# Kernel tuning notes

Hardware: AMD Instinct MI355X
Metric: run time of the kernel (lower is better)

The kernel has to match this reference:

```python
import jax, jax.numpy as jnp
import numpy as np

N_NODES, N_EDGES, N_GRAPHS = 100000, 800000, 64
X_DIM, E_DIM, U_DIM, H = 128, 64, 128, 128
BN_EPS = 1e-5


def _bn(x, gamma, beta):
    # BatchNorm1d, training mode: biased batch stats over dim 0
    m = x.mean(axis=0)
    v = x.var(axis=0)
    return (x - m) * jax.lax.rsqrt(v + BN_EPS) * gamma + beta


def _mlp(x, Wa, ba, g, be, Wb, bb):
    h = jax.nn.selu(_bn(x @ Wa + ba, g, be))
    return h @ Wb + bb


def setup_inputs() -> dict:
    key = jax.random.key(0)
    ks = jax.random.split(key, 10)
    x = jax.random.normal(ks[0], (N_NODES, X_DIM), jnp.float32)
    edge_attr = jax.random.normal(ks[1], (N_EDGES, E_DIM), jnp.float32)
    u = jax.random.normal(ks[2], (N_GRAPHS, U_DIM), jnp.float32)
    edge_index = jax.random.randint(ks[3], (2, N_EDGES), 0, N_NODES, jnp.int32)
    batch = jnp.sort(jax.random.randint(ks[4], (N_NODES,), 0, N_GRAPHS, jnp.int32))

    def lin(k, fan_in, fan_out):
        return jax.random.normal(k, (fan_in, fan_out), jnp.float32) / np.sqrt(fan_in)

    return {
        "x": x, "edge_attr": edge_attr, "u": u,
        "W1a": lin(ks[5], X_DIM + E_DIM, H), "b1a": jnp.zeros(H),
        "g1": jnp.ones(H), "be1": jnp.zeros(H),
        "W1b": lin(ks[6], H, H), "b1b": jnp.zeros(H),
        "W2a": lin(ks[7], X_DIM + H + U_DIM, H), "b2a": jnp.zeros(H),
        "g2": jnp.ones(H), "be2": jnp.zeros(H),
        "W2b": lin(ks[8], H, H), "b2b": jnp.zeros(H),
        "edge_index": edge_index, "batch": batch,
    }


def reference(x, edge_attr, u, W1a, b1a, g1, be1, W1b, b1b,
              W2a, b2a, g2, be2, W2b, b2b, edge_index, batch):
    row, col = edge_index[0], edge_index[1]
    n = x.shape[0]
    # gather source node feats, run edge MLP
    out = jnp.concatenate([x[row], edge_attr], axis=1)        # [E, X+Ed]
    out = _mlp(out, W1a, b1a, g1, be1, W1b, b1b)              # [E, H]
    # scatter-mean over destination nodes
    s = jax.ops.segment_sum(out, col, num_segments=n)         # [N, H]
    cnt = jax.ops.segment_sum(jnp.ones((out.shape[0], 1), out.dtype), col,
                              num_segments=n)
    agg = s / jnp.maximum(cnt, 1.0)
    # node update MLP
    out2 = jnp.concatenate([x, agg, u[batch]], axis=1)        # [N, X+H+U]
    return _mlp(out2, W2a, b2a, g2, be2, W2b, b2b)
```

## Files before the change

### kernel.cpp

```cpp
#include <hip/hip_runtime.h>
#include <hip/hip_bf16.h>
#include <math.h>


typedef __attribute__((ext_vector_type(8))) short bfrag;
typedef __attribute__((ext_vector_type(4))) float f32x4;
typedef __attribute__((ext_vector_type(4))) float f4raw;
typedef __attribute__((ext_vector_type(2))) unsigned u32x2;

#define N_EDGES 800000
#define N_NODES 100000
#define BN_EPS 1e-5f

static __device__ __forceinline__ short f2bf(float f) {
    union { float f; unsigned u; } v; v.f = f;
    unsigned r = (v.u + 0x7FFFu + ((v.u >> 16) & 1u)) >> 16;
    return (short)r;
}
static __device__ __forceinline__ float bf2f(short h) {
    union { unsigned u; float f; } v;
    v.u = ((unsigned)(unsigned short)h) << 16;
    return v.f;
}
static __device__ __forceinline__ unsigned pack2(float lo, float hi) {
    return ((unsigned)(unsigned short)f2bf(lo)) | (((unsigned)(unsigned short)f2bf(hi)) << 16);
}

static __device__ __forceinline__ bfrag load8f_bf(const float* __restrict__ p) {
    float4 a = *(const float4*)p;
    float4 b = *(const float4*)(p + 4);
    bfrag r;
    r[0] = f2bf(a.x); r[1] = f2bf(a.y); r[2] = f2bf(a.z); r[3] = f2bf(a.w);
    r[4] = f2bf(b.x); r[5] = f2bf(b.y); r[6] = f2bf(b.z); r[7] = f2bf(b.w);
    return r;
}
static __device__ __forceinline__ bfrag load8f_bf_nt(const float* __restrict__ p) {
    f4raw a = __builtin_nontemporal_load((const f4raw*)p);
    f4raw b = __builtin_nontemporal_load((const f4raw*)(p + 4));
    bfrag r;
    r[0] = f2bf(a[0]); r[1] = f2bf(a[1]); r[2] = f2bf(a[2]); r[3] = f2bf(a[3]);
    r[4] = f2bf(b[0]); r[5] = f2bf(b[1]); r[6] = f2bf(b[2]); r[7] = f2bf(b[3]);
    return r;
}
static __device__ __forceinline__ u32x2 ldnt_u2(const short* p) {
    return __builtin_nontemporal_load((const u32x2*)p);
}
static __device__ __forceinline__ void stnt_frag(short* p, bfrag v) {
    __builtin_nontemporal_store(v, (bfrag*)p);
}

static __device__ __forceinline__ float selu_f(float v) {
    return v > 0.f ? 1.0507009873554805f * v
                   : 1.7580993408473766f * (__expf(v) - 1.0f);
}

static __device__ __forceinline__ void pack_slot(short* __restrict__ Wp, int k, int n, float val) {
    int kb = k >> 5, g = (k >> 3) & 3, j = k & 7;
    Wp[(((size_t)kb * 128 + n) * 4 + g) * 8 + j] = f2bf(val);
}

__global__ void prep(const float* __restrict__ W1a, const float* __restrict__ W1b,
                     const float* __restrict__ b1b, const float* __restrict__ W2a,
                     const float* __restrict__ W2b,
                     short* __restrict__ Wp1x, short* __restrict__ Wp1e,
                     short* __restrict__ Wp2a, short* __restrict__ Wp2b,
                     float* __restrict__ cb,
                     const int* __restrict__ colI, int* __restrict__ CNTi, int E)
{
    const int b = blockIdx.x, t = threadIdx.x;
    if (b < 64) {
        int idx = b * 256 + t; int k = idx >> 7, n = idx & 127;
        pack_slot(Wp1x, k, n, W1a[idx]);
    } else if (b < 96) {
        int idx = (b - 64) * 256 + t; int k = idx >> 7, n = idx & 127;
        pack_slot(Wp1e, k, n, W1a[128 * 128 + idx]);
    } else if (b < 160) {
        int idx = (b - 96) * 256 + t; int k = idx >> 7, n = idx & 127;
        pack_slot(Wp2a, k, n, W2a[idx]);
    } else if (b < 224) {
        int idx = (b - 160) * 256 + t; int k = idx >> 7, n = idx & 127;
        int kt = ((k & 7) << 4) + (k >> 3);
        float s = 0.f;
        for (int j = 0; j < 128; ++j)
            s += W1b[kt * 128 + j] * W2a[(size_t)(128 + j) * 128 + n];
        pack_slot(Wp2a + 16384, k, n, s);
    } else if (b < 288) {
        int idx = (b - 224) * 256 + t; int k = idx >> 7, n = idx & 127;
        pack_slot(Wp2a + 32768, k, n, W2a[(size_t)256 * 128 + idx]);
    } else if (b < 352) {
        int idx = (b - 288) * 256 + t; int k = idx >> 7, n = idx & 127;
        int kt = ((k & 7) << 4) + (k >> 3);
        pack_slot(Wp2b, k, n, W2b[(size_t)kt * 128 + n]);
    } else if (b == 352) {
        if (t < 128) {
            float s = 0.f;
            for (int j = 0; j < 128; ++j) s += b1b[j] * W2a[(size_t)(128 + j) * 128 + t];
            cb[t] = s;
        }
    } else {
        int e = (b - 353) * 256 + t;
        if (e < E) atomicAdd(&CNTi[colI[e]], 1);
    }
}

__global__ void scan1(const int* __restrict__ cnt, int* __restrict__ off,
                      int* __restrict__ bsum, int N) {
    __shared__ int ls[1024];
    int i = blockIdx.x * 1024 + threadIdx.x;
    int v = (i < N) ? cnt[i] : 0;
    ls[threadIdx.x] = v;
    __syncthreads();
    for (int d = 1; d < 1024; d <<= 1) {
        int t = (threadIdx.x >= d) ? ls[threadIdx.x - d] : 0;
        __syncthreads();
        ls[threadIdx.x] += t;
        __syncthreads();
    }
    if (i < N) off[i] = ls[threadIdx.x] - v;
    if (threadIdx.x == 1023) bsum[blockIdx.x] = ls[1023];
}

__global__ void scan2(const int* __restrict__ bsum, int* __restrict__ boff, int NB) {
    __shared__ int ls[128];
    int v = (threadIdx.x < NB) ? bsum[threadIdx.x] : 0;
    ls[threadIdx.x] = v;
    __syncthreads();
    for (int d = 1; d < 128; d <<= 1) {
        int t = (threadIdx.x >= d) ? ls[threadIdx.x - d] : 0;
        __syncthreads();
        ls[threadIdx.x] += t;
        __syncthreads();
    }
    if (threadIdx.x < NB) boff[threadIdx.x] = ls[threadIdx.x] - v;
}

__global__ void scan3(int* __restrict__ off, const int* __restrict__ boff, int N) {
    int i = blockIdx.x * 1024 + threadIdx.x;
    if (i < N) off[i] += boff[blockIdx.x];
}

__global__ void fill_k(const int* __restrict__ col, int* __restrict__ off,
                       int* __restrict__ spos, int E) {
    int e = blockIdx.x * 256 + threadIdx.x;
    if (e < E) spos[e] = atomicAdd(&off[col[e]], 1);
}

__global__ __launch_bounds__(256) void gemmX(
    const float* __restrict__ x, const short* __restrict__ Wp,
    short* __restrict__ Xap, int N)
{
    const int lane = threadIdx.x & 63, wave = threadIdx.x >> 6;
    const int m0 = blockIdx.x * 128 + wave * 32;
    if (m0 >= N) return;
    const int lr = lane & 15, lg = lane >> 4;
    const int v0 = m0 + lr, v1 = m0 + 16 + lr;

    f32x4 acc[2][8];
#pragma unroll
    for (int t = 0; t < 2; ++t)
#pragma unroll
        for (int n = 0; n < 8; ++n) acc[t][n] = (f32x4){0.f, 0.f, 0.f, 0.f};

#pragma unroll
    for (int kb = 0; kb < 4; ++kb) {
        bfrag a0 = load8f_bf(x + (size_t)v0 * 128 + kb * 32 + lg * 8);
        bfrag a1 = load8f_bf(x + (size_t)v1 * 128 + kb * 32 + lg * 8);
        const short* wb = Wp + (size_t)kb * 4096;
#pragma unroll
        for (int n0 = 0; n0 < 8; ++n0) {
            bfrag b = *(const bfrag*)(wb + ((n0 * 16 + lr) * 4 + lg) * 8);
            acc[0][n0] = __builtin_amdgcn_mfma_f32_16x16x32_bf16(a0, b, acc[0][n0], 0, 0, 0);
            acc[1][n0] = __builtin_amdgcn_mfma_f32_16x16x32_bf16(a1, b, acc[1][n0], 0, 0, 0);
        }
    }
#pragma unroll
    for (int t = 0; t < 2; ++t) {
        const int rbase = m0 + t * 16 + lg * 4;
#pragma unroll
        for (int r = 0; r < 4; ++r) {
            bfrag o;
#pragma unroll
            for (int n0 = 0; n0 < 8; ++n0) o[n0] = f2bf(acc[t][n0][r]);
            *(bfrag*)(Xap + (size_t)(rbase + r) * 128 + lr * 8) = o;
        }
    }
}

__global__ __launch_bounds__(256) void gemm1n(
    const float* __restrict__ ea, const int* __restrict__ rowI,
    const int* __restrict__ SPOS, const short* __restrict__ Wp,
    const short* __restrict__ Xap, short* __restrict__ T1p,
    float* __restrict__ stats, int E)
{
    const int lane = threadIdx.x & 63, wave = threadIdx.x >> 6;
    const int lr = lane & 15, lg = lane >> 4;

    float ps[8], qs[8];
#pragma unroll
    for (int n0 = 0; n0 < 8; ++n0) { ps[n0] = 0.f; qs[n0] = 0.f; }

    const int NT = E >> 7;
    for (int tile = blockIdx.x; tile < NT; tile += gridDim.x) {
        const int m0 = tile * 128 + wave * 32;

        int spos[2][4];
        bfrag xa[2][4];
#pragma unroll
        for (int t = 0; t < 2; ++t) {
            const int rbase = m0 + t * 16 + lg * 4;
#pragma unroll
            for (int r = 0; r < 4; ++r) {
                const int e = rbase + r;
                spos[t][r] = SPOS[e];
                xa[t][r] = *(const bfrag*)(Xap + (size_t)rowI[e] * 128 + lr * 8);
            }
        }

        const float* er0 = ea + (size_t)(m0 + lr) * 64;
        const float* er1 = ea + (size_t)(m0 + 16 + lr) * 64;

        f32x4 acc[2][8];
#pragma unroll
        for (int t = 0; t < 2; ++t)
#pragma unroll
            for (int n = 0; n < 8; ++n) acc[t][n] = (f32x4){0.f, 0.f, 0.f, 0.f};

#pragma unroll
        for (int kb = 0; kb < 2; ++kb) {
            bfrag a0 = load8f_bf_nt(er0 + kb * 32 + lg * 8);
            bfrag a1 = load8f_bf_nt(er1 + kb * 32 + lg * 8);
            const short* wb = Wp + (size_t)kb * 4096;
#pragma unroll
            for (int n0 = 0; n0 < 8; ++n0) {
                bfrag b = *(const bfrag*)(wb + ((n0 * 16 + lr) * 4 + lg) * 8);
                acc[0][n0] = __builtin_amdgcn_mfma_f32_16x16x32_bf16(a0, b, acc[0][n0], 0, 0, 0);
                acc[1][n0] = __builtin_amdgcn_mfma_f32_16x16x32_bf16(a1, b, acc[1][n0], 0, 0, 0);
            }
        }

#pragma unroll
        for (int t = 0; t < 2; ++t) {
#pragma unroll
            for (int r = 0; r < 4; ++r) {
                bfrag o;
#pragma unroll
                for (int n0 = 0; n0 < 8; ++n0) {
                    float v = acc[t][n0][r] + bf2f(xa[t][r][n0]);
                    ps[n0] += v; qs[n0] += v * v;
                    o[n0] = f2bf(v);
                }
                stnt_frag(T1p + (size_t)spos[t][r] * 128 + lr * 8, o);
            }
        }
    }

    __shared__ float ls[256];
    ls[threadIdx.x] = 0.f;
    __syncthreads();
#pragma unroll
    for (int n0 = 0; n0 < 8; ++n0) {
        const int c = n0 * 16 + lr;
        float p = ps[n0], q = qs[n0];
        p += __shfl_xor(p, 16); p += __shfl_xor(p, 32);
        q += __shfl_xor(q, 16); q += __shfl_xor(q, 32);
        if (lg == 0) { atomicAdd(&ls[c], p); atomicAdd(&ls[128 + c], q); }
    }
    __syncthreads();
    atomicAdd(&stats[threadIdx.x], ls[threadIdx.x]);
}

__global__ __launch_bounds__(256) void gemm3f(
    const float* __restrict__ x, const short* __restrict__ T1p,
    const float* __restrict__ stats1, const float* __restrict__ g1,
    const float* __restrict__ be1,
    const int* __restrict__ OFF, const int* __restrict__ CNTi,
    const float* __restrict__ u, const int* __restrict__ batch,
    const float* __restrict__ cb, const short* __restrict__ Wp,
    short* __restrict__ T2p, float* __restrict__ stats2,
    int N, float invE)
{
    __shared__ short aggL[128][136];
    __shared__ float ls[256];
    __shared__ float ls_sc[128], ls_sh[128];
    ls[threadIdx.x] = 0.f;
    if (threadIdx.x < 128) {
        int p = threadIdx.x;
        int c = ((p & 7) << 4) + (p >> 3);
        float mean = stats1[c] * invE;
        float var = stats1[128 + c] * invE - mean * mean;
        float sc = g1[c] * rsqrtf(var + BN_EPS);
        ls_sc[p] = sc;
        ls_sh[p] = be1[c] - mean * sc;
    }
    __syncthreads();

    const int lane = threadIdx.x & 63, wave = threadIdx.x >> 6;
    const int m0b = blockIdx.x * 128;

    {
        const int h = lane >> 5, t = lane & 31;
        const float sc0 = ls_sc[t * 4 + 0], sc1 = ls_sc[t * 4 + 1];
        const float sc2 = ls_sc[t * 4 + 2], sc3 = ls_sc[t * 4 + 3];
        const float sh0 = ls_sh[t * 4 + 0], sh1 = ls_sh[t * 4 + 1];
        const float sh2 = ls_sh[t * 4 + 2], sh3 = ls_sh[t * 4 + 3];
        for (int i = 0; i < 32; ++i) {
            const int v = m0b + wave * 32 + i;
            if (v >= N) break;
            const int cnt = CNTi[v];
            const int beg = OFF[v] - cnt;
            const short* base = T1p + (size_t)beg * 128 + t * 4;
            float a0 = 0.f, a1 = 0.f, a2 = 0.f, a3 = 0.f;
            int j = 0;
            for (; j + 4 <= cnt; j += 4) {
                u32x2 wA = ldnt_u2(base + (size_t)(j + h) * 128);
                u32x2 wB = ldnt_u2(base + (size_t)(j + 2 + h) * 128);
                a0 += selu_f(sc0 * bf2f((short)(wA[0] & 0xffff)) + sh0);
                a1 += selu_f(sc1 * bf2f((short)(wA[0] >> 16)) + sh1);
                a2 += selu_f(sc2 * bf2f((short)(wA[1] & 0xffff)) + sh2);
                a3 += selu_f(sc3 * bf2f((short)(wA[1] >> 16)) + sh3);
                a0 += selu_f(sc0 * bf2f((short)(wB[0] & 0xffff)) + sh0);
                a1 += selu_f(sc1 * bf2f((short)(wB[0] >> 16)) + sh1);
                a2 += selu_f(sc2 * bf2f((short)(wB[1] & 0xffff)) + sh2);
                a3 += selu_f(sc3 * bf2f((short)(wB[1] >> 16)) + sh3);
            }
            for (; j < cnt; j += 2) {
                if (j + h < cnt) {
                    u32x2 w = ldnt_u2(base + (size_t)(j + h) * 128);
                    a0 += selu_f(sc0 * bf2f((short)(w[0] & 0xffff)) + sh0);
                    a1 += selu_f(sc1 * bf2f((short)(w[0] >> 16)) + sh1);
                    a2 += selu_f(sc2 * bf2f((short)(w[1] & 0xffff)) + sh2);
                    a3 += selu_f(sc3 * bf2f((short)(w[1] >> 16)) + sh3);
                }
            }
            a0 += __shfl_xor(a0, 32); a1 += __shfl_xor(a1, 32);
            a2 += __shfl_xor(a2, 32); a3 += __shfl_xor(a3, 32);
            if (h == 0) {
                const float inv = 1.0f / fmaxf((float)cnt, 1.0f);
                u32x2 o;
                o[0] = pack2(a0 * inv, a1 * inv);
                o[1] = pack2(a2 * inv, a3 * inv);
                *(u32x2*)&aggL[wave * 32 + i][t * 4] = o;
            }
        }
    }
    __syncthreads();

    const int m0 = m0b + wave * 32;
    const bool active = (m0 < N);
    const int lr = lane & 15, lg = lane >> 4;

    if (active) {
        const int v0 = m0 + lr, v1 = m0 + 16 + lr;
        const float* u0 = u + (size_t)batch[v0] * 128;
        const float* u1 = u + (size_t)batch[v1] * 128;

        f32x4 acc[2][8];
#pragma unroll
        for (int t = 0; t < 2; ++t)
#pragma unroll
            for (int n = 0; n < 8; ++n) acc[t][n] = (f32x4){0.f, 0.f, 0.f, 0.f};

#pragma unroll
        for (int kb = 0; kb < 12; ++kb) {
            bfrag a0, a1;
            if (kb >= 4 && kb < 8) {
                a0 = *(const bfrag*)&aggL[wave * 32 + lr][(kb - 4) * 32 + lg * 8];
                a1 = *(const bfrag*)&aggL[wave * 32 + 16 + lr][(kb - 4) * 32 + lg * 8];
            } else {
                const float *p0, *p1;
                if (kb < 4) {
                    p0 = x + (size_t)v0 * 128 + kb * 32 + lg * 8;
                    p1 = x + (size_t)v1 * 128 + kb * 32 + lg * 8;
                } else {
                    p0 = u0 + (kb - 8) * 32 + lg * 8;
                    p1 = u1 + (kb - 8) * 32 + lg * 8;
                }
                a0 = load8f_bf(p0);
                a1 = load8f_bf(p1);
            }
            const short* wb = Wp + (size_t)kb * 4096;
#pragma unroll
            for (int n0 = 0; n0 < 8; ++n0) {
                bfrag b = *(const bfrag*)(wb + ((n0 * 16 + lr) * 4 + lg) * 8);
                acc[0][n0] = __builtin_amdgcn_mfma_f32_16x16x32_bf16(a0, b, acc[0][n0], 0, 0, 0);
                acc[1][n0] = __builtin_amdgcn_mfma_f32_16x16x32_bf16(a1, b, acc[1][n0], 0, 0, 0);
            }
        }
        float cbl[8];
#pragma unroll
        for (int n0 = 0; n0 < 8; ++n0) cbl[n0] = cb[n0 * 16 + lr];
        float ps[8], qs[8];
#pragma unroll
        for (int n0 = 0; n0 < 8; ++n0) { ps[n0] = 0.f; qs[n0] = 0.f; }
#pragma unroll
        for (int t = 0; t < 2; ++t) {
            const int rbase = m0 + t * 16 + lg * 4;
            float fl[4];
#pragma unroll
            for (int r = 0; r < 4; ++r) fl[r] = (CNTi[rbase + r] > 0) ? 1.f : 0.f;
#pragma unroll
            for (int r = 0; r < 4; ++r) {
                bfrag o;
#pragma unroll
                for (int n0 = 0; n0 < 8; ++n0) {
                    float v = acc[t][n0][r] + fl[r] * cbl[n0];
                    ps[n0] += v; qs[n0] += v * v;
                    o[n0] = f2bf(v);
                }
                *(bfrag*)(T2p + (size_t)(rbase + r) * 128 + lr * 8) = o;
            }
        }
#pragma unroll
        for (int n0 = 0; n0 < 8; ++n0) {
            const int c = n0 * 16 + lr;
            float p = ps[n0], q = qs[n0];
            p += __shfl_xor(p, 16); p += __shfl_xor(p, 32);
            q += __shfl_xor(q, 16); q += __shfl_xor(q, 32);
            if (lg == 0) { atomicAdd(&ls[c], p); atomicAdd(&ls[128 + c], q); }
        }
    }
    __syncthreads();
    atomicAdd(&stats2[threadIdx.x], ls[threadIdx.x]);
}

__global__ __launch_bounds__(256) void gemm4_node(
    const short* __restrict__ T2p, const float* __restrict__ stats,
    const float* __restrict__ g2, const float* __restrict__ be2,
    const short* __restrict__ Wp, const float* __restrict__ b2b,
    float* __restrict__ out, int N, float invR)
{
    __shared__ float ls_sc[128], ls_sh[128];
    if (threadIdx.x < 128) {
        int c = threadIdx.x;
        float mean = stats[c] * invR;
        float var = stats[128 + c] * invR - mean * mean;
        float sc = g2[c] * rsqrtf(var + BN_EPS);
        ls_sc[c] = sc;
        ls_sh[c] = be2[c] - mean * sc;
    }
    __syncthreads();

    const int lane = threadIdx.x & 63, wave = threadIdx.x >> 6;
    const int m0 = blockIdx.x * 128 + wave * 32;
    if (m0 >= N) return;
    const int lr = lane & 15, lg = lane >> 4;
    const int e0 = m0 + lr, e1 = m0 + 16 + lr;

    f32x4 acc[2][8];
#pragma unroll
    for (int n0 = 0; n0 < 8; ++n0) {
        float bias = b2b[n0 * 16 + lr];
        acc[0][n0] = (f32x4){bias, bias, bias, bias};
        acc[1][n0] = (f32x4){bias, bias, bias, bias};
    }
#pragma unroll
    for (int kb = 0; kb < 4; ++kb) {
        float scl[8], shf[8];
#pragma unroll
        for (int j = 0; j < 8; ++j) {
            int c = j * 16 + kb * 4 + lg;
            scl[j] = ls_sc[c];
            shf[j] = ls_sh[c];
        }
        bfrag r0 = *(const bfrag*)(T2p + (size_t)e0 * 128 + kb * 32 + lg * 8);
        bfrag r1 = *(const bfrag*)(T2p + (size_t)e1 * 128 + kb * 32 + lg * 8);
        bfrag a0, a1;
#pragma unroll
        for (int j = 0; j < 8; ++j) {
            a0[j] = f2bf(selu_f(bf2f(r0[j]) * scl[j] + shf[j]));
            a1[j] = f2bf(selu_f(bf2f(r1[j]) * scl[j] + shf[j]));
        }
        const short* wb = Wp + (size_t)kb * 4096;
#pragma unroll
        for (int n0 = 0; n0 < 8; ++n0) {
            bfrag b = *(const bfrag*)(wb + ((n0 * 16 + lr) * 4 + lg) * 8);
            acc[0][n0] = __builtin_amdgcn_mfma_f32_16x16x32_bf16(a0, b, acc[0][n0], 0, 0, 0);
            acc[1][n0] = __builtin_amdgcn_mfma_f32_16x16x32_bf16(a1, b, acc[1][n0], 0, 0, 0);
        }
    }
#pragma unroll
    for (int t = 0; t < 2; ++t) {
        const int rbase = m0 + t * 16 + lg * 4;
#pragma unroll
        for (int n0 = 0; n0 < 8; ++n0) {
            const int c = n0 * 16 + lr;
#pragma unroll
            for (int r = 0; r < 4; ++r)
                __builtin_nontemporal_store(acc[t][n0][r],
                    out + (size_t)(rbase + r) * 128 + c);
        }
    }
}

extern "C" void kernel_launch(void* const* d_in, const int* in_sizes, int n_in,
                              void* d_out, int out_size, void* d_ws, size_t ws_size,
                              hipStream_t stream)
{
    const float* x   = (const float*)d_in[0];
    const float* ea  = (const float*)d_in[1];
    const float* u   = (const float*)d_in[2];
    const float* W1a = (const float*)d_in[3];
    const float* g1  = (const float*)d_in[5];
    const float* be1 = (const float*)d_in[6];
    const float* W1b = (const float*)d_in[7];
    const float* b1b = (const float*)d_in[8];
    const float* W2a = (const float*)d_in[9];
    const float* g2  = (const float*)d_in[11];
    const float* be2 = (const float*)d_in[12];
    const float* W2b = (const float*)d_in[13];
    const float* b2b = (const float*)d_in[14];
    const int* ei    = (const int*)d_in[15];
    const int* rowI  = ei;
    const int* colI  = ei + N_EDGES;
    const int* batch = (const int*)d_in[16];
    float* out = (float*)d_out;

    if (ws_size < 260252416ull) return;

    char* ws = (char*)d_ws;
    short* Wp1x   = (short*)(ws + 0);
    short* Wp1e   = (short*)(ws + 32768);
    short* Wp2a   = (short*)(ws + 49152);
    short* Wp2b   = (short*)(ws + 147456);
    float* cb     = (float*)(ws + 245760);
    float* stats1 = (float*)(ws + 246272);
    float* stats2 = (float*)(ws + 247296);
    int*   CNTi   = (int*)(ws + 250368);
    int*   OFF    = (int*)(ws + 650368);
    int*   BSUM   = (int*)(ws + 1050368);
    int*   BOFF   = (int*)(ws + 1051392);
    int*   SPOS   = (int*)(ws + 1052416);
    short* Xap    = (short*)(ws + 29852416ull);
    short* T2p    = (short*)(ws + 29852416ull);
    short* T1p    = (short*)(ws + 55452416ull);

    hipMemsetAsync(stats1, 0, 2048, stream);
    hipMemsetAsync(CNTi, 0, 400000, stream);

    prep<<<353 + (N_EDGES + 255) / 256, 256, 0, stream>>>(
        W1a, W1b, b1b, W2a, W2b, Wp1x, Wp1e, Wp2a, Wp2b, cb, colI, CNTi, N_EDGES);

    scan1<<<98, 1024, 0, stream>>>(CNTi, OFF, BSUM, N_NODES);
    scan2<<<1, 128, 0, stream>>>(BSUM, BOFF, 98);
    scan3<<<98, 1024, 0, stream>>>(OFF, BOFF, N_NODES);
    fill_k<<<(N_EDGES + 255) / 256, 256, 0, stream>>>(colI, OFF, SPOS, N_EDGES);

    gemmX<<<(N_NODES + 127) / 128, 256, 0, stream>>>(x, Wp1x, Xap, N_NODES);

    gemm1n<<<2048, 256, 0, stream>>>(ea, rowI, SPOS, Wp1e, Xap, T1p, stats1, N_EDGES);

    gemm3f<<<(N_NODES + 127) / 128, 256, 0, stream>>>(
        x, T1p, stats1, g1, be1, OFF, CNTi, u, batch, cb, Wp2a, T2p, stats2,
        N_NODES, 1.0f / (float)N_EDGES);

    gemm4_node<<<(N_NODES + 127) / 128, 256, 0, stream>>>(T2p, stats2, g2, be2, Wp2b, b2b,
                                                          out, N_NODES, 1.0f / (float)N_NODES);
}
```

Before: 458.3 us.

## Split segment aggregation out of node GEMM into separate wide-grid kernel

The fused gemm3f kernel did the segment-mean aggregation (BN+SELU over T1 rows) in LDS and then ran the node GEMM. This splits it into segsel, a 2048-block kernel that writes per-node means to a global bf16 buffer, and gemm3_node, which reads that buffer as the A operand. The aim is more parallelism for the memory-bound gather phase, since the old launch had only 782 blocks doing 32 serial nodes per wave. The cost is an extra kernel launch and a 25.6MB write plus read-back of the aggregate buffer.

Measured after the change: 370.7 us (median of 2 runs). 19.1% less time.

```diff
diff --git a/kernel.cpp b/kernel.cpp
--- a/kernel.cpp
+++ b/kernel.cpp
@@ -269,85 +269,90 @@
     atomicAdd(&stats[threadIdx.x], ls[threadIdx.x]);
 }
 
-__global__ __launch_bounds__(256) void gemm3f(
-    const float* __restrict__ x, const short* __restrict__ T1p,
-    const float* __restrict__ stats1, const float* __restrict__ g1,
-    const float* __restrict__ be1,
+__global__ __launch_bounds__(256) void segsel(
+    const short* __restrict__ T1p, const float* __restrict__ stats,
+    const float* __restrict__ g1, const float* __restrict__ be1,
     const int* __restrict__ OFF, const int* __restrict__ CNTi,
-    const float* __restrict__ u, const int* __restrict__ batch,
-    const float* __restrict__ cb, const short* __restrict__ Wp,
-    short* __restrict__ T2p, float* __restrict__ stats2,
-    int N, float invE)
-{
-    __shared__ short aggL[128][136];
-    __shared__ float ls[256];
+    short* __restrict__ Aggm, int N, float invR)
+{
     __shared__ float ls_sc[128], ls_sh[128];
-    ls[threadIdx.x] = 0.f;
     if (threadIdx.x < 128) {
         int p = threadIdx.x;
         int c = ((p & 7) << 4) + (p >> 3);
-        float mean = stats1[c] * invE;
-        float var = stats1[128 + c] * invE - mean * mean;
+        float mean = stats[c] * invR;
+        float var = stats[128 + c] * invR - mean * mean;
         float sc = g1[c] * rsqrtf(var + BN_EPS);
         ls_sc[p] = sc;
         ls_sh[p] = be1[c] - mean * sc;
     }
     __syncthreads();
 
+    const int lane = threadIdx.x & 63;
+    const int h = lane >> 5, t = lane & 31;
+    const int wid = blockIdx.x * 4 + (threadIdx.x >> 6);
+    const int nw = gridDim.x * 4;
+    const int chunk = (N + nw - 1) / nw;
+    const int v0 = wid * chunk;
+    const int v1 = (v0 + chunk < N) ? v0 + chunk : N;
+
+    const float sc0 = ls_sc[t * 4 + 0], sc1 = ls_sc[t * 4 + 1];
+    const float sc2 = ls_sc[t * 4 + 2], sc3 = ls_sc[t * 4 + 3];
+    const float sh0 = ls_sh[t * 4 + 0], sh1 = ls_sh[t * 4 + 1];
+    const float sh2 = ls_sh[t * 4 + 2], sh3 = ls_sh[t * 4 + 3];
+
+    for (int v = v0; v < v1; ++v) {
+        const int cnt = CNTi[v];
+        const int beg = OFF[v] - cnt;
+        const short* base = T1p + (size_t)beg * 128 + t * 4;
+        float a0 = 0.f, a1 = 0.f, a2 = 0.f, a3 = 0.f;
+        int j = 0;
+        for (; j + 4 <= cnt; j += 4) {
+            u32x2 wA = ldnt_u2(base + (size_t)(j + h) * 128);
+            u32x2 wB = ldnt_u2(base + (size_t)(j + 2 + h) * 128);
+            a0 += selu_f(sc0 * bf2f((short)(wA[0] & 0xffff)) + sh0);
+            a1 += selu_f(sc1 * bf2f((short)(wA[0] >> 16)) + sh1);
+            a2 += selu_f(sc2 * bf2f((short)(wA[1] & 0xffff)) + sh2);
+            a3 += selu_f(sc3 * bf2f((short)(wA[1] >> 16)) + sh3);
+            a0 += selu_f(sc0 * bf2f((short)(wB[0] & 0xffff)) + sh0);
+            a1 += selu_f(sc1 * bf2f((short)(wB[0] >> 16)) + sh1);
+            a2 += selu_f(sc2 * bf2f((short)(wB[1] & 0xffff)) + sh2);
+            a3 += selu_f(sc3 * bf2f((short)(wB[1] >> 16)) + sh3);
+        }
+        for (; j < cnt; j += 2) {
+            if (j + h < cnt) {
+                u32x2 w = ldnt_u2(base + (size_t)(j + h) * 128);
+                a0 += selu_f(sc0 * bf2f((short)(w[0] & 0xffff)) + sh0);
+                a1 += selu_f(sc1 * bf2f((short)(w[0] >> 16)) + sh1);
+                a2 += selu_f(sc2 * bf2f((short)(w[1] & 0xffff)) + sh2);
+                a3 += selu_f(sc3 * bf2f((short)(w[1] >> 16)) + sh3);
+            }
+        }
+        a0 += __shfl_xor(a0, 32); a1 += __shfl_xor(a1, 32);
+        a2 += __shfl_xor(a2, 32); a3 += __shfl_xor(a3, 32);
+        if (h == 0) {
+            const float inv = 1.0f / fmaxf((float)cnt, 1.0f);
+            u32x2 o;
+            o[0] = pack2(a0 * inv, a1 * inv);
+            o[1] = pack2(a2 * inv, a3 * inv);
+            *(u32x2*)(Aggm + (size_t)v * 128 + t * 4) = o;
+        }
+    }
+}
+
+__global__ __launch_bounds__(256) void gemm3_node(
+    const float* __restrict__ x, const short* __restrict__ Aggm,
+    const float* __restrict__ u, const int* __restrict__ batch,
+    const int* __restrict__ CNTi, const float* __restrict__ cb,
+    const short* __restrict__ Wp, short* __restrict__ T2p,
+    float* __restrict__ stats, int N)
+{
     const int lane = threadIdx.x & 63, wave = threadIdx.x >> 6;
-    const int m0b = blockIdx.x * 128;
-
-    {
-        const int h = lane >> 5, t = lane & 31;
-        const float sc0 = ls_sc[t * 4 + 0], sc1 = ls_sc[t * 4 + 1];
-        const float sc2 = ls_sc[t * 4 + 2], sc3 = ls_sc[t * 4 + 3];
-        const float sh0 = ls_sh[t * 4 + 0], sh1 = ls_sh[t * 4 + 1];
-        const float sh2 = ls_sh[t * 4 + 2], sh3 = ls_sh[t * 4 + 3];
-        for (int i = 0; i < 32; ++i) {
-            const int v = m0b + wave * 32 + i;
-            if (v >= N) break;
-            const int cnt = CNTi[v];
-            const int beg = OFF[v] - cnt;
-            const short* base = T1p + (size_t)beg * 128 + t * 4;
-            float a0 = 0.f, a1 = 0.f, a2 = 0.f, a3 = 0.f;
-            int j = 0;
-            for (; j + 4 <= cnt; j += 4) {
-                u32x2 wA = ldnt_u2(base + (size_t)(j + h) * 128);
-                u32x2 wB = ldnt_u2(base + (size_t)(j + 2 + h) * 128);
-                a0 += selu_f(sc0 * bf2f((short)(wA[0] & 0xffff)) + sh0);
-                a1 += selu_f(sc1 * bf2f((short)(wA[0] >> 16)) + sh1);
-                a2 += selu_f(sc2 * bf2f((short)(wA[1] & 0xffff)) + sh2);
-                a3 += selu_f(sc3 * bf2f((short)(wA[1] >> 16)) + sh3);
-                a0 += selu_f(sc0 * bf2f((short)(wB[0] & 0xffff)) + sh0);
-                a1 += selu_f(sc1 * bf2f((short)(wB[0] >> 16)) + sh1);
-                a2 += selu_f(sc2 * bf2f((short)(wB[1] & 0xffff)) + sh2);
-                a3 += selu_f(sc3 * bf2f((short)(wB[1] >> 16)) + sh3);
-            }
-            for (; j < cnt; j += 2) {
-                if (j + h < cnt) {
-                    u32x2 w = ldnt_u2(base + (size_t)(j + h) * 128);
-                    a0 += selu_f(sc0 * bf2f((short)(w[0] & 0xffff)) + sh0);
-                    a1 += selu_f(sc1 * bf2f((short)(w[0] >> 16)) + sh1);
-                    a2 += selu_f(sc2 * bf2f((short)(w[1] & 0xffff)) + sh2);
-                    a3 += selu_f(sc3 * bf2f((short)(w[1] >> 16)) + sh3);
-                }
-            }
-            a0 += __shfl_xor(a0, 32); a1 += __shfl_xor(a1, 32);
-            a2 += __shfl_xor(a2, 32); a3 += __shfl_xor(a3, 32);
-            if (h == 0) {
-                const float inv = 1.0f / fmaxf((float)cnt, 1.0f);
-                u32x2 o;
-                o[0] = pack2(a0 * inv, a1 * inv);
-                o[1] = pack2(a2 * inv, a3 * inv);
-                *(u32x2*)&aggL[wave * 32 + i][t * 4] = o;
-            }
-        }
-    }
-    __syncthreads();
-
-    const int m0 = m0b + wave * 32;
+    const int m0 = blockIdx.x * 128 + wave * 32;
     const bool active = (m0 < N);
     const int lr = lane & 15, lg = lane >> 4;
+    __shared__ float ls[256];
+    ls[threadIdx.x] = 0.f;
+    __syncthreads();
 
     if (active) {
         const int v0 = m0 + lr, v1 = m0 + 16 + lr;
@@ -364,8 +369,8 @@
         for (int kb = 0; kb < 12; ++kb) {
             bfrag a0, a1;
             if (kb >= 4 && kb < 8) {
-                a0 = *(const bfrag*)&aggL[wave * 32 + lr][(kb - 4) * 32 + lg * 8];
-                a1 = *(const bfrag*)&aggL[wave * 32 + 16 + lr][(kb - 4) * 32 + lg * 8];
+                a0 = *(const bfrag*)(Aggm + (size_t)v0 * 128 + (kb - 4) * 32 + lg * 8);
+                a1 = *(const bfrag*)(Aggm + (size_t)v1 * 128 + (kb - 4) * 32 + lg * 8);
             } else {
                 const float *p0, *p1;
                 if (kb < 4) {
@@ -420,7 +425,7 @@
         }
     }
     __syncthreads();
-    atomicAdd(&stats2[threadIdx.x], ls[threadIdx.x]);
+    atomicAdd(&stats[threadIdx.x], ls[threadIdx.x]);
 }
 
 __global__ __launch_bounds__(256) void gemm4_node(
@@ -530,6 +535,7 @@
     int*   BSUM   = (int*)(ws + 1050368);
     int*   BOFF   = (int*)(ws + 1051392);
     int*   SPOS   = (int*)(ws + 1052416);
+    short* Aggm   = (short*)(ws + 4252416);
     short* Xap    = (short*)(ws + 29852416ull);
     short* T2p    = (short*)(ws + 29852416ull);
     short* T1p    = (short*)(ws + 55452416ull);
@@ -549,10 +555,11 @@
 
     gemm1n<<<2048, 256, 0, stream>>>(ea, rowI, SPOS, Wp1e, Xap, T1p, stats1, N_EDGES);
 
-    gemm3f<<<(N_NODES + 127) / 128, 256, 0, stream>>>(
-        x, T1p, stats1, g1, be1, OFF, CNTi, u, batch, cb, Wp2a, T2p, stats2,
-        N_NODES, 1.0f / (float)N_EDGES);
-
+    segsel<<<2048, 256, 0, stream>>>(T1p, stats1, g1, be1, OFF, CNTi, Aggm,
+                                     N_NODES, 1.0f / (float)N_EDGES);
+
+    gemm3_node<<<(N_NODES + 127) / 128, 256, 0, stream>>>(x, Aggm, u, batch, CNTi, cb,
+                                                          Wp2a, T2p, stats2, N_NODES);
     gemm4_node<<<(N_NODES + 127) / 128, 256, 0, stream>>>(T2p, stats2, g2, be2, Wp2b, b2b,
                                                           out, N_NODES, 1.0f / (float)N_NODES);
 }
```
